# Kernel tuning notes

Hardware: AMD Instinct MI355X
Metric: run time of the kernel (lower is better)

## Reference

```python
import jax, jax.numpy as jnp
import numpy as np

K = 5
TAU = 0.5
N = 8192
IN_DIM = 128
OUT_DIM = 128


def setup_inputs() -> dict:
    key = jax.random.key(0)
    k1, k2, k3 = jax.random.split(key, 3)
    x = jax.random.normal(k1, (N, IN_DIM), dtype=jnp.float32)
    laplacian = jax.random.normal(k2, (N, N), dtype=jnp.float32) / np.sqrt(N)
    # xavier-uniform-like init for theta (K, in_dim, out_dim)
    limit = np.sqrt(6.0 / (IN_DIM + OUT_DIM))
    theta = jax.random.uniform(k3, (K, IN_DIM, OUT_DIM), dtype=jnp.float32,
                               minval=-limit, maxval=limit)
    return {"x": x, "laplacian": laplacian, "theta": theta}


def _cheb_coeff(k_order: int, tau: float) -> jnp.ndarray:
    # c_k = (2/K) * exp(-tau * cos(pi*(k+0.5)/K)), Chebyshev-Gauss nodes
    ks = jnp.arange(k_order, dtype=jnp.float32)
    x_k = jnp.cos(jnp.pi * (ks + 0.5) / k_order)
    return (2.0 / k_order) * jnp.exp(-tau * x_k)


def reference(x, laplacian, theta):
    coeff = _cheb_coeff(K, TAU)  # (K,)
    # Chebyshev recurrence: T_0 = x, T_1 = L x, T_k = 2 L T_{k-1} - T_{k-2}
    tx_prev, tx_curr = x, laplacian @ x
    tx_list = [tx_prev, tx_curr]
    for _ in range(2, K):
        tx_next = 2.0 * (laplacian @ tx_curr) - tx_prev
        tx_list.append(tx_next)
        tx_prev, tx_curr = tx_curr, tx_next
    tx_stack = jnp.stack(tx_list, axis=0)  # (K, N, in_dim)
    return jnp.einsum('kni,kio,k->no', tx_stack, theta, coeff)
```

## Files before the change

### kernel.cpp

```cpp
#include <hip/hip_runtime.h>
#include <hip/hip_bf16.h>
#include <cmath>

#define NROWS 8192
#define DIM   128
#define KDIM  8192
#define BM    64
#define BN    128
#define BK    64
#define SPLITK 4
#define KCHUNK (KDIM / SPLITK)
#define GITERS (KCHUNK / BK)
#define MTILES (NROWS / BM)
#define KBLKS  (KDIM / BK)
#define NBUF   3
#define LDSTRIDE 80

typedef __bf16 bf16_t;
typedef __bf16 bf16x8 __attribute__((ext_vector_type(8)));
typedef float  f32x4  __attribute__((ext_vector_type(4)));


__device__ __forceinline__ void async16(const void* g, void* l) {
    __builtin_amdgcn_global_load_lds(
        (const __attribute__((address_space(1))) unsigned int*)g,
        (__attribute__((address_space(3))) unsigned int*)l, 16, 0, 0);
}

__global__ void k_theta(const float* __restrict__ th, bf16_t* __restrict__ out,
                        float c0, float c1, float c2, float c3, float c4) {
    int idx = blockIdx.x * 256 + threadIdx.x;
    int k = idx >> 14;
    int o = (idx >> 7) & 127;
    int i = idx & 127;
    float c = (k == 0) ? c0 : (k == 1) ? c1 : (k == 2) ? c2 : (k == 3) ? c3 : c4;
    out[idx] = (bf16_t)(c * th[(k << 14) + (i << 7) + o]);
}

__global__ __launch_bounds__(256)
void k_convert(const float* __restrict__ L, bf16_t* __restrict__ Lbf) {
    const int lane = threadIdx.x & 63;
    const int lrow = lane >> 3;
    const int p    = lane & 7;
    const int c    = p ^ lrow;
    const int nWaves = gridDim.x * 4;
    const int TOT = (NROWS / 8) * KBLKS;
    for (int w = blockIdx.x * 4 + (threadIdx.x >> 6); w < TOT; w += nWaves) {
        const int rg   = w >> 7;
        const int kblk = w & (KBLKS - 1);
        const int row  = rg * 8 + lrow;
        const float* src = L + (size_t)row * KDIM + kblk * 64 + c * 8;
        float4 a = *(const float4*)src;
        float4 b = *(const float4*)(src + 4);
        bf16x8 v;
        v[0] = (bf16_t)a.x; v[1] = (bf16_t)a.y; v[2] = (bf16_t)a.z; v[3] = (bf16_t)a.w;
        v[4] = (bf16_t)b.x; v[5] = (bf16_t)b.y; v[6] = (bf16_t)b.z; v[7] = (bf16_t)b.w;
        *(bf16x8*)(Lbf + (((size_t)rg * KBLKS + kblk) * 64 + lane) * 8) = v;
    }
}

__global__ __launch_bounds__(256, 2)
void k_gemm(const bf16_t* __restrict__ A, const bf16_t* __restrict__ Bt,
            float* __restrict__ partial) {
    __shared__ __align__(16) bf16_t As[NBUF][BM * BK];
    __shared__ __align__(16) bf16_t Bs[NBUF][BN * BK];

    const int t     = threadIdx.x;
    const int mTile = blockIdx.x & (MTILES - 1);
    const int s     = blockIdx.x >> 7;
    const int mb    = mTile * BM;
    const int sKB   = s * (KCHUNK / BK);
    const int rgA   = mb >> 3;
    const int wave = t >> 6, lane = t & 63;
    const int wM = (wave & 1) * 32;
    const int wN = (wave >> 1) * 64;
    const int lm = lane & 15, lk = lane >> 4;

    f32x4 acc[2][4];
#pragma unroll
    for (int a = 0; a < 2; ++a)
#pragma unroll
        for (int b = 0; b < 4; ++b) acc[a][b] = (f32x4)0.0f;

    auto stage = [&](int kk, int buf) {
        const int kblk = sKB + kk;
#pragma unroll
        for (int j = 0; j < 2; ++j) {
            const int rg = rgA + wave * 2 + j;
            async16(A + (((size_t)rg * KBLKS + kblk) * 64 + lane) * 8,
                    &As[buf][(wave * 16 + j * 8) * BK]);
        }
#pragma unroll
        for (int i = 0; i < 4; ++i) {
            const int fg = wave * 4 + i;
            async16(Bt + (((size_t)fg * KBLKS + kblk) * 64 + lane) * 8,
                    &Bs[buf][(wave * 32 + i * 8) * BK]);
        }
    };

    auto compute = [&](int buf) {
#pragma unroll
        for (int ko = 0; ko < 2; ++ko) {
            const int csX = (ko * 4 + lk) ^ (lm & 7);
            bf16x8 af[2], bfr[4];
#pragma unroll
            for (int tm = 0; tm < 2; ++tm)
                af[tm] = *(const bf16x8*)(&As[buf][(wM + tm * 16 + lm) * BK + csX * 8]);
#pragma unroll
            for (int tn = 0; tn < 4; ++tn)
                bfr[tn] = *(const bf16x8*)(&Bs[buf][(wN + tn * 16 + lm) * BK + csX * 8]);
            __builtin_amdgcn_s_setprio(1);
#pragma unroll
            for (int tm = 0; tm < 2; ++tm)
#pragma unroll
                for (int tn = 0; tn < 4; ++tn)
                    acc[tm][tn] = __builtin_amdgcn_mfma_f32_16x16x32_bf16(
                        af[tm], bfr[tn], acc[tm][tn], 0, 0, 0);
            __builtin_amdgcn_s_setprio(0);
        }
    };

    stage(0, 0); stage(1, 1); stage(2, 2);

    for (int kk = 0; kk < GITERS - 2; ++kk) {
        const int buf = kk % NBUF;
        asm volatile("s_waitcnt vmcnt(12)" ::: "memory");
        __builtin_amdgcn_s_barrier();
        __builtin_amdgcn_sched_barrier(0);
        compute(buf);
        __builtin_amdgcn_sched_barrier(0);
        __builtin_amdgcn_s_barrier();
        if (kk < GITERS - 3) stage(kk + 3, buf);
    }
    asm volatile("s_waitcnt vmcnt(6)" ::: "memory");
    __builtin_amdgcn_s_barrier();
    __builtin_amdgcn_sched_barrier(0);
    compute((GITERS - 2) % NBUF);
    asm volatile("s_waitcnt vmcnt(0)" ::: "memory");
    __builtin_amdgcn_s_barrier();
    __builtin_amdgcn_sched_barrier(0);
    compute((GITERS - 1) % NBUF);

    float* pOut = partial + (size_t)s * NROWS * DIM;
#pragma unroll
    for (int tm = 0; tm < 2; ++tm)
#pragma unroll
        for (int tn = 0; tn < 4; ++tn)
#pragma unroll
            for (int r = 0; r < 4; ++r) {
                const int row = mb + wM + tm * 16 + lk * 4 + r;
                const int col = wN + tn * 16 + lm;
                pOut[(size_t)row * DIM + col] = acc[tm][tn][r];
            }
}

template <int MODE>
__global__ void k_combine(const float* __restrict__ src, const float* __restrict__ prev,
                          float* __restrict__ f32dst, bf16_t* __restrict__ tbf,
                          bf16_t* __restrict__ bt) {
    __shared__ bf16_t tl[128 * 24];
    const size_t S = (size_t)NROWS * DIM;
    const int t  = threadIdx.x;
    const int n0 = blockIdx.x * 16;
    const int nl = t >> 4;
    const int dp = (t & 15) * 8;
    const int n  = n0 + nl;

    float y[8];
    if (MODE == 0) {
        float4 a = *(const float4*)(src + (size_t)n * DIM + dp);
        float4 b = *(const float4*)(src + (size_t)n * DIM + dp + 4);
        y[0] = a.x; y[1] = a.y; y[2] = a.z; y[3] = a.w;
        y[4] = b.x; y[5] = b.y; y[6] = b.z; y[7] = b.w;
    } else {
#pragma unroll
        for (int j = 0; j < 8; ++j) y[j] = 0.0f;
#pragma unroll
        for (int ss = 0; ss < SPLITK; ++ss) {
            const float* p = src + (size_t)ss * S + (size_t)n * DIM + dp;
            float4 a = *(const float4*)p;
            float4 b = *(const float4*)(p + 4);
            y[0] += a.x; y[1] += a.y; y[2] += a.z; y[3] += a.w;
            y[4] += b.x; y[5] += b.y; y[6] += b.z; y[7] += b.w;
        }
        if (MODE == 2) {
            float4 a = *(const float4*)(prev + (size_t)n * DIM + dp);
            float4 b = *(const float4*)(prev + (size_t)n * DIM + dp + 4);
            y[0] = 2.0f * y[0] - a.x; y[1] = 2.0f * y[1] - a.y;
            y[2] = 2.0f * y[2] - a.z; y[3] = 2.0f * y[3] - a.w;
            y[4] = 2.0f * y[4] - b.x; y[5] = 2.0f * y[5] - b.y;
            y[6] = 2.0f * y[6] - b.z; y[7] = 2.0f * y[7] - b.w;
        }
    }
    if (f32dst) {
        float4 a, b;
        a.x = y[0]; a.y = y[1]; a.z = y[2]; a.w = y[3];
        b.x = y[4]; b.y = y[5]; b.z = y[6]; b.w = y[7];
        *(float4*)(f32dst + (size_t)n * DIM + dp) = a;
        *(float4*)(f32dst + (size_t)n * DIM + dp + 4) = b;
    }
    bf16x8 v;
#pragma unroll
    for (int j = 0; j < 8; ++j) v[j] = (bf16_t)y[j];
    *(bf16x8*)(tbf + (size_t)n * DIM + dp) = v;
    if (bt) {
#pragma unroll
        for (int j = 0; j < 8; ++j) tl[(dp + j) * 24 + nl] = v[j];
        __syncthreads();
        const int d = t >> 1;
        const int h = (t & 1) * 8;
        bf16x8 w = *(const bf16x8*)(&tl[d * 24 + h]);
        const int c    = ((n0 + h) >> 3) & 7;
        const int lane = (d & 7) * 8 + (c ^ (d & 7));
        const size_t a16 = ((size_t)(d >> 3) * KBLKS + (n0 >> 6)) * 64 + lane;
        *(bf16x8*)(bt + a16 * 8) = w;
    }
}

__global__ __launch_bounds__(256, 2)
void k_proj(const bf16_t* __restrict__ T, const bf16_t* __restrict__ W,
            float* __restrict__ out) {
    __shared__ __align__(16) bf16_t As[64 * LDSTRIDE];
    __shared__ __align__(16) bf16_t Bs[128 * LDSTRIDE];

    const int t  = threadIdx.x;
    const int mb = blockIdx.x * 64;
    const int wave = t >> 6, lane = t & 63;
    const int wM = (wave & 1) * 32;
    const int wN = (wave >> 1) * 64;
    const int lm = lane & 15, lk = lane >> 4;
    const int arow = t >> 3;
    const int asc  = t & 7;
    const size_t S = (size_t)NROWS * DIM;

    f32x4 acc[2][4];
#pragma unroll
    for (int a = 0; a < 2; ++a)
#pragma unroll
        for (int b = 0; b < 4; ++b) acc[a][b] = (f32x4)0.0f;

    bf16x8 aR[2], bR[4];

    auto loadT = [&](int it) {
        const int seg = it >> 1;
        const int h   = (it & 1) * 64;
#pragma unroll
        for (int rep = 0; rep < 2; ++rep) {
            const int r = rep * 32 + arow;
            aR[rep] = *(const bf16x8*)(T + (size_t)seg * S +
                        (size_t)(mb + r) * DIM + h + asc * 8);
        }
#pragma unroll
        for (int rep = 0; rep < 4; ++rep) {
            const int o = rep * 32 + arow;
            bR[rep] = *(const bf16x8*)(W + seg * 16384 + o * 128 + h + asc * 8);
        }
    };
    auto storeT = [&]() {
#pragma unroll
        for (int rep = 0; rep < 2; ++rep) {
            const int r = rep * 32 + arow;
            *(bf16x8*)(&As[r * LDSTRIDE + asc * 8]) = aR[rep];
        }
#pragma unroll
        for (int rep = 0; rep < 4; ++rep) {
            const int o = rep * 32 + arow;
            *(bf16x8*)(&Bs[o * LDSTRIDE + asc * 8]) = bR[rep];
        }
    };

    loadT(0);
    for (int it = 0; it < 10; ++it) {
        __syncthreads();
        storeT();
        __syncthreads();
        if (it + 1 < 10) loadT(it + 1);
#pragma unroll
        for (int ko = 0; ko < 2; ++ko) {
            bf16x8 af[2], bfr[4];
#pragma unroll
            for (int tm = 0; tm < 2; ++tm)
                af[tm] = *(const bf16x8*)(&As[(wM + tm * 16 + lm) * LDSTRIDE +
                                              (ko * 4 + lk) * 8]);
#pragma unroll
            for (int tn = 0; tn < 4; ++tn)
                bfr[tn] = *(const bf16x8*)(&Bs[(wN + tn * 16 + lm) * LDSTRIDE +
                                               (ko * 4 + lk) * 8]);
#pragma unroll
            for (int tm = 0; tm < 2; ++tm)
#pragma unroll
                for (int tn = 0; tn < 4; ++tn)
                    acc[tm][tn] = __builtin_amdgcn_mfma_f32_16x16x32_bf16(
                        af[tm], bfr[tn], acc[tm][tn], 0, 0, 0);
        }
    }
#pragma unroll
    for (int tm = 0; tm < 2; ++tm)
#pragma unroll
        for (int tn = 0; tn < 4; ++tn)
#pragma unroll
            for (int r = 0; r < 4; ++r) {
                const int row = mb + wM + tm * 16 + lk * 4 + r;
                const int col = wN + tn * 16 + lm;
                out[(size_t)row * DIM + col] = acc[tm][tn][r];
            }
}

extern "C" void kernel_launch(void* const* d_in, const int* in_sizes, int n_in,
                              void* d_out, int out_size, void* d_ws, size_t ws_size,
                              hipStream_t stream) {
    const float* x  = nullptr;
    const float* L  = nullptr;
    const float* th = nullptr;
    for (int i = 0; i < n_in; ++i) {
        if (in_sizes[i] == NROWS * KDIM)       L  = (const float*)d_in[i];
        else if (in_sizes[i] == NROWS * DIM)   x  = (const float*)d_in[i];
        else if (in_sizes[i] == 5 * DIM * DIM) th = (const float*)d_in[i];
    }
    float* out = (float*)d_out;

    const size_t S = (size_t)NROWS * DIM;
    char* ws = (char*)d_ws;
    size_t off = 0;
    auto alloc = [&](size_t bytes) {
        void* p = ws + off;
        off = (off + bytes + 255) & ~(size_t)255;
        return p;
    };
    bf16_t* Tbf     = (bf16_t*)alloc(5 * S * 2);
    bf16_t* Bt      = (bf16_t*)alloc(5 * S * 2);
    float*  Tf32    = (float*)alloc(2 * S * 4);
    bf16_t* thT     = (bf16_t*)alloc(5 * 128 * 128 * 2);
    float*  partial = (float*)alloc((size_t)SPLITK * S * 4);
    bf16_t* Lbf     = (bf16_t*)alloc((size_t)NROWS * KDIM * 2);
    if (off > ws_size) return;

    float c[5];
    for (int k = 0; k < 5; ++k)
        c[k] = (float)((2.0 / 5.0) * exp(-0.5 * cos(M_PI * (k + 0.5) / 5.0)));

    dim3 blk(256);
    k_theta<<<320, blk, 0, stream>>>(th, thT, c[0], c[1], c[2], c[3], c[4]);
    k_convert<<<2048, blk, 0, stream>>>(L, Lbf);
    k_combine<0><<<512, blk, 0, stream>>>(x, nullptr, nullptr, Tbf, Bt);

    for (int j = 1; j <= 4; ++j) {
        const bf16_t* Bj = Bt + (size_t)(j - 1) * S;
        k_gemm<<<MTILES * SPLITK, blk, 0, stream>>>(Lbf, Bj, partial);
        bf16_t* tbf = Tbf + (size_t)j * S;
        bf16_t* bt  = (j < 4) ? Bt + (size_t)j * S : nullptr;
        if (j == 1)
            k_combine<1><<<512, blk, 0, stream>>>(partial, nullptr, Tf32 + S, tbf, bt);
        else if (j == 2)
            k_combine<2><<<512, blk, 0, stream>>>(partial, x, Tf32, tbf, bt);
        else if (j == 3)
            k_combine<2><<<512, blk, 0, stream>>>(partial, Tf32 + S, Tf32 + S, tbf, bt);
        else
            k_combine<2><<<512, blk, 0, stream>>>(partial, Tf32, nullptr, tbf, nullptr);
    }
    k_proj<<<128, blk, 0, stream>>>(Tbf, thT, out);
}
```

Before: 560.2 us.

## Retile Laplacian GEMM to 128-row tiles, BK32, split-K 8, fragment-native layouts

The GEMM is reworked to 512-thread blocks, each computing a 128x128 tile with K steps of 32, eight-way split-K and a four-deep async LDS buffer ring. The converted Laplacian and the transposed B operand are written in a 16x32 fragment-native image, so each wave issues a single 16-byte async load per operand per stage and reads MFMA fragments without XOR swizzling. Block indexing now puts the split index in the low bits, and the pipeline prologue and epilogue are rewritten for the deeper ring. In exchange, split-K partial output doubles, which adds store traffic in the GEMM and read traffic in the combine kernel.

```diff
diff --git a/kernel.cpp b/kernel.cpp
--- a/kernel.cpp
+++ b/kernel.cpp
@@ -5,15 +5,16 @@
 #define NROWS 8192
 #define DIM   128
 #define KDIM  8192
-#define BM    64
+#define BM    128
 #define BN    128
-#define BK    64
-#define SPLITK 4
+#define BK    32
+#define SPLITK 8
 #define KCHUNK (KDIM / SPLITK)
 #define GITERS (KCHUNK / BK)
 #define MTILES (NROWS / BM)
-#define KBLKS  (KDIM / BK)
-#define NBUF   3
+#define KB32   (KDIM / 32)
+#define NB32   (NROWS / 32)
+#define NBUF   4
 #define LDSTRIDE 80
 
 typedef __bf16 bf16_t;
@@ -38,43 +39,40 @@
 }
 
 __global__ __launch_bounds__(256)
-void k_convert(const float* __restrict__ L, bf16_t* __restrict__ Lbf) {
+void k_convert(const float* __restrict__ L, bf16_t* __restrict__ img) {
     const int lane = threadIdx.x & 63;
-    const int lrow = lane >> 3;
-    const int p    = lane & 7;
-    const int c    = p ^ lrow;
-    const int nWaves = gridDim.x * 4;
-    const int TOT = (NROWS / 8) * KBLKS;
-    for (int w = blockIdx.x * 4 + (threadIdx.x >> 6); w < TOT; w += nWaves) {
-        const int rg   = w >> 7;
-        const int kblk = w & (KBLKS - 1);
-        const int row  = rg * 8 + lrow;
-        const float* src = L + (size_t)row * KDIM + kblk * 64 + c * 8;
+    const int p = lane >> 4, lrow = lane & 15;
+    const int wid = blockIdx.x * 4 + (threadIdx.x >> 6);
+    const int nW = gridDim.x * 4;
+    const int TOT = (NROWS / 16) * KB32;
+    for (int u = wid; u < TOT; u += nW) {
+        const int rg = u >> 8;
+        const int kblk = u & (KB32 - 1);
+        const float* src = L + (size_t)(rg * 16 + lrow) * KDIM + kblk * 32 + p * 8;
         float4 a = *(const float4*)src;
         float4 b = *(const float4*)(src + 4);
         bf16x8 v;
         v[0] = (bf16_t)a.x; v[1] = (bf16_t)a.y; v[2] = (bf16_t)a.z; v[3] = (bf16_t)a.w;
         v[4] = (bf16_t)b.x; v[5] = (bf16_t)b.y; v[6] = (bf16_t)b.z; v[7] = (bf16_t)b.w;
-        *(bf16x8*)(Lbf + (((size_t)rg * KBLKS + kblk) * 64 + lane) * 8) = v;
-    }
-}
-
-__global__ __launch_bounds__(256, 2)
+        *(bf16x8*)(img + (((size_t)rg * KB32 + kblk) * 64 + lane) * 8) = v;
+    }
+}
+
+__global__ __launch_bounds__(512, 4)
 void k_gemm(const bf16_t* __restrict__ A, const bf16_t* __restrict__ Bt,
             float* __restrict__ partial) {
     __shared__ __align__(16) bf16_t As[NBUF][BM * BK];
     __shared__ __align__(16) bf16_t Bs[NBUF][BN * BK];
 
     const int t     = threadIdx.x;
-    const int mTile = blockIdx.x & (MTILES - 1);
-    const int s     = blockIdx.x >> 7;
+    const int s     = blockIdx.x & (SPLITK - 1);
+    const int mTile = blockIdx.x >> 3;
     const int mb    = mTile * BM;
-    const int sKB   = s * (KCHUNK / BK);
-    const int rgA   = mb >> 3;
     const int wave = t >> 6, lane = t & 63;
-    const int wM = (wave & 1) * 32;
-    const int wN = (wave >> 1) * 64;
+    const int wM = (wave & 3) * 32;
+    const int wN = (wave >> 2) * 64;
     const int lm = lane & 15, lk = lane >> 4;
+    const int kb0 = s * (KCHUNK / 32);
 
     f32x4 acc[2][4];
 #pragma unroll
@@ -83,63 +81,59 @@
         for (int b = 0; b < 4; ++b) acc[a][b] = (f32x4)0.0f;
 
     auto stage = [&](int kk, int buf) {
-        const int kblk = sKB + kk;
-#pragma unroll
-        for (int j = 0; j < 2; ++j) {
-            const int rg = rgA + wave * 2 + j;
-            async16(A + (((size_t)rg * KBLKS + kblk) * 64 + lane) * 8,
-                    &As[buf][(wave * 16 + j * 8) * BK]);
-        }
-#pragma unroll
-        for (int i = 0; i < 4; ++i) {
-            const int fg = wave * 4 + i;
-            async16(Bt + (((size_t)fg * KBLKS + kblk) * 64 + lane) * 8,
-                    &Bs[buf][(wave * 32 + i * 8) * BK]);
-        }
+        const int kblk = kb0 + kk;
+        async16(A + (((size_t)((mb >> 4) + wave) * KB32 + kblk) * 64 + lane) * 8,
+                &As[buf][wave * 512]);
+        async16(Bt + (((size_t)wave * NB32 + kblk) * 64 + lane) * 8,
+                &Bs[buf][wave * 512]);
     };
 
     auto compute = [&](int buf) {
-#pragma unroll
-        for (int ko = 0; ko < 2; ++ko) {
-            const int csX = (ko * 4 + lk) ^ (lm & 7);
-            bf16x8 af[2], bfr[4];
-#pragma unroll
-            for (int tm = 0; tm < 2; ++tm)
-                af[tm] = *(const bf16x8*)(&As[buf][(wM + tm * 16 + lm) * BK + csX * 8]);
+        bf16x8 af[2], bfr[4];
+#pragma unroll
+        for (int tm = 0; tm < 2; ++tm)
+            af[tm] = *(const bf16x8*)(&As[buf][((wM >> 4) + tm) * 512 + lk * 128 + lm * 8]);
+#pragma unroll
+        for (int tn = 0; tn < 4; ++tn)
+            bfr[tn] = *(const bf16x8*)(&Bs[buf][((wN >> 4) + tn) * 512 + lk * 128 + lm * 8]);
+        __builtin_amdgcn_s_setprio(1);
+#pragma unroll
+        for (int tm = 0; tm < 2; ++tm)
 #pragma unroll
             for (int tn = 0; tn < 4; ++tn)
-                bfr[tn] = *(const bf16x8*)(&Bs[buf][(wN + tn * 16 + lm) * BK + csX * 8]);
-            __builtin_amdgcn_s_setprio(1);
-#pragma unroll
-            for (int tm = 0; tm < 2; ++tm)
-#pragma unroll
-                for (int tn = 0; tn < 4; ++tn)
-                    acc[tm][tn] = __builtin_amdgcn_mfma_f32_16x16x32_bf16(
-                        af[tm], bfr[tn], acc[tm][tn], 0, 0, 0);
-            __builtin_amdgcn_s_setprio(0);
-        }
-    };
-
-    stage(0, 0); stage(1, 1); stage(2, 2);
-
-    for (int kk = 0; kk < GITERS - 2; ++kk) {
-        const int buf = kk % NBUF;
-        asm volatile("s_waitcnt vmcnt(12)" ::: "memory");
+                acc[tm][tn] = __builtin_amdgcn_mfma_f32_16x16x32_bf16(
+                    af[tm], bfr[tn], acc[tm][tn], 0, 0, 0);
+        __builtin_amdgcn_s_setprio(0);
+    };
+
+    stage(0, 0); stage(1, 1); stage(2, 2); stage(3, 3);
+
+    for (int kk = 0; kk < GITERS - 3; ++kk) {
+        const int buf = kk & 3;
+        asm volatile("s_waitcnt vmcnt(6)" ::: "memory");
         __builtin_amdgcn_s_barrier();
         __builtin_amdgcn_sched_barrier(0);
         compute(buf);
         __builtin_amdgcn_sched_barrier(0);
         __builtin_amdgcn_s_barrier();
-        if (kk < GITERS - 3) stage(kk + 3, buf);
-    }
-    asm volatile("s_waitcnt vmcnt(6)" ::: "memory");
-    __builtin_amdgcn_s_barrier();
-    __builtin_amdgcn_sched_barrier(0);
-    compute((GITERS - 2) % NBUF);
+        if (kk + 4 < GITERS) stage(kk + 4, buf);
+    }
+    asm volatile("s_waitcnt vmcnt(4)" ::: "memory");
+    __builtin_amdgcn_s_barrier();
+    __builtin_amdgcn_sched_barrier(0);
+    compute((GITERS - 3) & 3);
+    __builtin_amdgcn_sched_barrier(0);
+    __builtin_amdgcn_s_barrier();
+    asm volatile("s_waitcnt vmcnt(2)" ::: "memory");
+    __builtin_amdgcn_s_barrier();
+    __builtin_amdgcn_sched_barrier(0);
+    compute((GITERS - 2) & 3);
+    __builtin_amdgcn_sched_barrier(0);
+    __builtin_amdgcn_s_barrier();
     asm volatile("s_waitcnt vmcnt(0)" ::: "memory");
     __builtin_amdgcn_s_barrier();
     __builtin_amdgcn_sched_barrier(0);
-    compute((GITERS - 1) % NBUF);
+    compute((GITERS - 1) & 3);
 
     float* pOut = partial + (size_t)s * NROWS * DIM;
 #pragma unroll
@@ -210,9 +204,9 @@
         const int d = t >> 1;
         const int h = (t & 1) * 8;
         bf16x8 w = *(const bf16x8*)(&tl[d * 24 + h]);
-        const int c    = ((n0 + h) >> 3) & 7;
-        const int lane = (d & 7) * 8 + (c ^ (d & 7));
-        const size_t a16 = ((size_t)(d >> 3) * KBLKS + (n0 >> 6)) * 64 + lane;
+        const int nn = n0 + h;
+        const size_t a16 = ((size_t)(d >> 4) * NB32 + (nn >> 5)) * 64 +
+                           ((nn >> 3) & 3) * 16 + (d & 15);
         *(bf16x8*)(bt + a16 * 8) = w;
     }
 }
@@ -346,7 +340,7 @@
 
     for (int j = 1; j <= 4; ++j) {
         const bf16_t* Bj = Bt + (size_t)(j - 1) * S;
-        k_gemm<<<MTILES * SPLITK, blk, 0, stream>>>(Lbf, Bj, partial);
+        k_gemm<<<MTILES * SPLITK, dim3(512), 0, stream>>>(Lbf, Bj, partial);
         bf16_t* tbf = Tbf + (size_t)j * S;
         bf16_t* bt  = (j < 4) ? Bt + (size_t)j * S : nullptr;
         if (j == 1)
```

After: 552.1 us. Within noise of the previous version (-1.4%).
